# Kernel tuning notes

Hardware: AMD Instinct MI355X
Metric: run time of the kernel (lower is better)

Reference implementation:

```python
import jax, jax.numpy as jnp
import numpy as np

B, S, D, H, FF = 8, 1024, 2048, 16, 8192
Dh = D // H
EPS = 1e-5

def _layernorm(x, g, b):
    m = jnp.mean(x, axis=-1, keepdims=True)
    v = jnp.mean(jnp.square(x - m), axis=-1, keepdims=True)
    return (x - m) / jnp.sqrt(v + EPS) * g + b

def setup_inputs() -> dict:
    key = jax.random.key(0)
    ks = jax.random.split(key, 12)
    sc_d = 1.0 / np.sqrt(D)
    sc_ff = 1.0 / np.sqrt(FF)
    return {
        "x": jax.random.normal(ks[0], (B, S, D), dtype=jnp.float32),
        "mask": jnp.ones((S, S), dtype=jnp.int32),
        "Wq": jax.random.normal(ks[1], (D, D), dtype=jnp.float32) * sc_d,
        "bq": jnp.zeros((D,), dtype=jnp.float32),
        "Wk": jax.random.normal(ks[2], (D, D), dtype=jnp.float32) * sc_d,
        "bk": jnp.zeros((D,), dtype=jnp.float32),
        "Wv": jax.random.normal(ks[3], (D, D), dtype=jnp.float32) * sc_d,
        "bv": jnp.zeros((D,), dtype=jnp.float32),
        "Wo": jax.random.normal(ks[4], (D, D), dtype=jnp.float32) * sc_d,
        "bo": jnp.zeros((D,), dtype=jnp.float32),
        "W1": jax.random.normal(ks[5], (FF, D), dtype=jnp.float32) * sc_d,
        "b1": jnp.zeros((FF,), dtype=jnp.float32),
        "W2": jax.random.normal(ks[6], (D, FF), dtype=jnp.float32) * sc_ff,
        "b2": jnp.zeros((D,), dtype=jnp.float32),
        "g1": jnp.ones((D,), dtype=jnp.float32),
        "be1": jnp.zeros((D,), dtype=jnp.float32),
        "g2": jnp.ones((D,), dtype=jnp.float32),
        "be2": jnp.zeros((D,), dtype=jnp.float32),
    }

def reference(x, mask, Wq, bq, Wk, bk, Wv, bv, Wo, bo, W1, b1, W2, b2, g1, be1, g2, be2):
    # --- multi-head attention (chunk along d_model == reshape to heads) ---
    q = (x @ Wq.T + bq).reshape(B, S, H, Dh)
    k = (x @ Wk.T + bk).reshape(B, S, H, Dh)
    v = (x @ Wv.T + bv).reshape(B, S, H, Dh)
    score = jnp.einsum('bqhd,bkhd->bhqk', q, k) / jnp.sqrt(jnp.float32(Dh))
    score = jnp.where(mask == 0, jnp.float32(-1e9), score)
    attn = jax.nn.softmax(score, axis=-1)
    out = jnp.einsum('bhqk,bkhd->bqhd', attn, v).reshape(B, S, D)
    attn_out = out @ Wo.T + bo
    # --- residual + post-LN ---
    x1 = _layernorm(attn_out + x, g1, be1)
    # --- FFN ---
    h = jax.nn.relu(x1 @ W1.T + b1)
    ffn_out = h @ W2.T + b2
    return _layernorm(ffn_out + x1, g2, be2)
```

## Files before the change

### kernel.cpp

```cpp
#include <hip/hip_runtime.h>
#include <cstdint>
#include <cstddef>


typedef unsigned short u16;
typedef unsigned int   u32;
typedef unsigned long long u64;
typedef __attribute__((ext_vector_type(8))) short short8;
typedef __attribute__((ext_vector_type(4))) float f32x4;

constexpr int Bc  = 8;
constexpr int Sc  = 1024;
constexpr int Dc  = 2048;
constexpr int Hc  = 16;
constexpr int Dhc = 128;
constexpr int FFc = 8192;
constexpr int Mc  = Bc * Sc;

__device__ __forceinline__ u16 f2b(float f) {
  u32 u = __builtin_bit_cast(u32, f);
  u += 0x7fffu + ((u >> 16) & 1u);
  return (u16)(u >> 16);
}
__device__ __forceinline__ u32 pack2(float a, float b) {
  return (u32)f2b(a) | ((u32)f2b(b) << 16);
}
__device__ __forceinline__ void unpack8(uint4 u, float* f) {
  u32 w[4] = {u.x, u.y, u.z, u.w};
#pragma unroll
  for (int i = 0; i < 4; ++i) {
    f[2 * i + 0] = __builtin_bit_cast(float, w[i] << 16);
    f[2 * i + 1] = __builtin_bit_cast(float, w[i] & 0xffff0000u);
  }
}

#define GLOAD_LDS16(gp, lp)                                                    \
  __builtin_amdgcn_global_load_lds(                                            \
      (const __attribute__((address_space(1))) void*)(gp),                     \
      (__attribute__((address_space(3))) void*)(lp), 16, 0, 0)

__global__ __launch_bounds__(256) void cvt_f32_bf16(const float* __restrict__ in,
                                                    u16* __restrict__ out, int n) {
  int i = (blockIdx.x * 256 + threadIdx.x) << 2;
  if (i >= n) return;
  float4 v = *(const float4*)(in + i);
  ushort4 o;
  o.x = f2b(v.x); o.y = f2b(v.y); o.z = f2b(v.z); o.w = f2b(v.w);
  *(ushort4*)(out + i) = o;
}

__global__ __launch_bounds__(256) void mask_bits(const int* __restrict__ mask,
                                                 u64* __restrict__ mb) {
  int t = blockIdx.x * 256 + threadIdx.x;
  int r = t >> 4, wd = t & 15;
  const int* p = mask + (size_t)r * Sc + wd * 64;
  u64 bits = 0;
#pragma unroll 16
  for (int i = 0; i < 64; i += 4) {
    int4 q = *(const int4*)(p + i);
    bits |= (u64)(q.x != 0) << (i + 0);
    bits |= (u64)(q.y != 0) << (i + 1);
    bits |= (u64)(q.z != 0) << (i + 2);
    bits |= (u64)(q.w != 0) << (i + 3);
  }
  mb[t] = bits;
}

template <int MODE>
__global__ __launch_bounds__(512, 2) void gemm256tb(const u16* __restrict__ A,
                                                    const u16* __restrict__ Bt,
                                                    const float* __restrict__ bias,
                                                    u16* __restrict__ C,
                                                    int M, int N, int K) {
  __shared__ u16 Abuf[4][256 * 32];
  __shared__ u16 Bbuf[4][256 * 32];

  const int nbn = N >> 8;
  const int nwg = (M >> 8) * nbn;
  int bid = blockIdx.x;
  int sw = (bid & 7) * (nwg >> 3) + (bid >> 3);
  const int m0 = (sw / nbn) << 8;
  const int n0 = (sw % nbn) << 8;

  const int tid  = threadIdx.x;
  const int lane = tid & 63;
  const int w    = tid >> 6;
  const int wm   = w >> 2;
  const int wn   = w & 3;

  const int rowA = lane & 15;
  const int g4   = lane >> 4;

  const int p16  = lane << 4;
  const int wsw  = p16 ^ (((p16 >> 9) & 1) << 5);
  const int s_rr = wsw >> 6;
  const int s_cc = (wsw & 63) >> 1;

  const int sb = (rowA * 64 + g4 * 16) ^ (((rowA >> 3) & 1) << 5);

  const int NT = K >> 5;

  const u16* Asrc = A  + (size_t)(m0 + w * 32 + s_rr) * K + s_cc;
  const u16* Bsrc = Bt + (size_t)(n0 + w * 32 + s_rr) * K + s_cc;

  auto stage = [&](int tt) {
    int buf = tt & 3;
#pragma unroll
    for (int i = 0; i < 2; ++i)
      GLOAD_LDS16(Asrc + (size_t)i * 16 * K + tt * 32, &Abuf[buf][(2 * w + i) * 512]);
#pragma unroll
    for (int i = 0; i < 2; ++i)
      GLOAD_LDS16(Bsrc + (size_t)i * 16 * K + tt * 32, &Bbuf[buf][(2 * w + i) * 512]);
  };

  auto readF = [&](int tt, short8* aF, short8* bF) {
    int buf = tt & 3;
#pragma unroll
    for (int n = 0; n < 4; ++n)
      bF[n] = *(const short8*)((const char*)&Bbuf[buf][(wn * 4 + n) * 512] + sb);
#pragma unroll
    for (int i = 0; i < 8; ++i)
      aF[i] = *(const short8*)((const char*)&Abuf[buf][(wm * 8 + i) * 512] + sb);
  };

  f32x4 acc[8][4];
#pragma unroll
  for (int m = 0; m < 8; ++m)
#pragma unroll
    for (int n = 0; n < 4; ++n) acc[m][n] = (f32x4){0.f, 0.f, 0.f, 0.f};

  stage(0); stage(1); stage(2);
  asm volatile("s_waitcnt vmcnt(4)" ::: "memory");
  __builtin_amdgcn_s_barrier();

  short8 a0[8], b0[4], a1[8], b1[4];
  readF(0, a0, b0);

  auto body = [&](int t, short8* aC, short8* bC, short8* aN, short8* bN) {
    if (t + 1 < NT) readF(t + 1, aN, bN);
    if (t + 3 < NT) stage(t + 3);
    __builtin_amdgcn_sched_barrier(0);
    __builtin_amdgcn_s_setprio(1);
#pragma unroll
    for (int i = 0; i < 8; ++i)
#pragma unroll
      for (int n = 0; n < 4; ++n)
        acc[i][n] = __builtin_amdgcn_mfma_f32_16x16x32_bf16(aC[i], bC[n], acc[i][n], 0, 0, 0);
    __builtin_amdgcn_s_setprio(0);
    if (t + 3 < NT) { asm volatile("s_waitcnt vmcnt(4)" ::: "memory"); }
    else            { asm volatile("s_waitcnt vmcnt(0)" ::: "memory"); }
    __builtin_amdgcn_s_barrier();
  };

  for (int t = 0; t < NT; t += 2) {
    body(t,     a0, b0, a1, b1);
    body(t + 1, a1, b1, a0, b0);
  }

  const int ci = lane & 15;
  const int ri = g4 << 2;
  float bvv[4];
#pragma unroll
  for (int n = 0; n < 4; ++n) bvv[n] = bias[n0 + wn * 64 + n * 16 + ci];

  if (MODE == 2) {
#pragma unroll
    for (int n = 0; n < 4; ++n) {
      int col = n0 + wn * 64 + n * 16 + ci;
#pragma unroll
      for (int m = 0; m < 8; ++m) {
        int row0 = m0 + wm * 128 + m * 16 + ri;
        ushort4 pk;
        pk.x = f2b(acc[m][n][0] + bvv[n]);
        pk.y = f2b(acc[m][n][1] + bvv[n]);
        pk.z = f2b(acc[m][n][2] + bvv[n]);
        pk.w = f2b(acc[m][n][3] + bvv[n]);
        size_t addr = ((size_t)((row0 >> 10) * Hc + (col >> 7)) * 128 + (col & 127)) * 1024
                      + (row0 & 1023);
        *(ushort4*)(C + addr) = pk;
      }
    }
  } else {
#pragma unroll
    for (int m = 0; m < 8; ++m) {
      int row0 = m0 + wm * 128 + m * 16 + ri;
#pragma unroll
      for (int j = 0; j < 4; ++j) {
        u16* cp = C + (size_t)(row0 + j) * N + n0 + wn * 64 + ci;
#pragma unroll
        for (int n = 0; n < 4; ++n) {
          float v = acc[m][n][j] + bvv[n];
          if (MODE == 1) v = fmaxf(v, 0.f);
          cp[n * 16] = f2b(v);
        }
      }
    }
  }
}

__global__ __launch_bounds__(256, 2) void attn_mfma(
    const u16* __restrict__ qb,
    const u16* __restrict__ kb,
    const u16* __restrict__ vt,
    const u64* __restrict__ mb,
    u16* __restrict__ ob)
{
  __shared__ u16 Ks[64 * 128];
  __shared__ u16 Vts[128 * 64];
  __shared__ u16 Ps[4][32 * 64];

  const int bid = blockIdx.x;
  const int l   = (bid & 7) * 128 + (bid >> 3);
  const int qt  = l & 7;
  const int bh  = l >> 3;
  const int h   = bh & (Hc - 1);
  const int b   = bh >> 4;
  const int q0  = qt * 128;

  const int tid  = threadIdx.x;
  const int lane = tid & 63;
  const int w    = tid >> 6;
  const int rowA = lane & 15;
  const int g4   = lane >> 4;
  const int kq16 = g4 << 3;
  const int ri   = g4 << 2;

  const size_t tokbase = (size_t)b * Sc * Dc + (size_t)h * Dhc;
  const size_t vtbase  = (size_t)bh * 128 * 1024;
  const int qwbase = q0 + w * 32;

  short8 qf[2][4];
#pragma unroll
  for (int m = 0; m < 2; ++m)
#pragma unroll
    for (int kk = 0; kk < 4; ++kk)
      qf[m][kk] = *reinterpret_cast<const short8*>(
          qb + tokbase + (size_t)(qwbase + m * 16 + rowA) * Dc + kk * 32 + kq16);

  f32x4 O[2][8];
#pragma unroll
  for (int m = 0; m < 2; ++m)
#pragma unroll
    for (int n = 0; n < 8; ++n) O[m][n] = (f32x4){0.f, 0.f, 0.f, 0.f};
  float mrow[2][4], lrow[2][4];
#pragma unroll
  for (int m = 0; m < 2; ++m)
#pragma unroll
    for (int j = 0; j < 4; ++j) { mrow[m][j] = -INFINITY; lrow[m][j] = 0.f; }

  const float scale = 0.08838834764831845f;

  for (int kt = 0; kt < Sc / 64; ++kt) {
    const int k0 = kt * 64;
    __syncthreads();
#pragma unroll
    for (int i = 0; i < 4; ++i) {
      int chunk = w * 4 + i;
      int gb = (chunk * 64 + lane) * 16;
      int L  = gb ^ (((gb >> 8) & 7) << 4);
      int row = L >> 8, ce = (L & 255) >> 1;
      GLOAD_LDS16(kb + tokbase + (size_t)(k0 + row) * Dc + ce, &Ks[chunk * 512]);
    }
#pragma unroll
    for (int i = 0; i < 4; ++i) {
      int chunk = w * 4 + i;
      int gb = (chunk * 64 + lane) * 16;
      int L  = gb ^ (((gb >> 7) & 7) << 4);
      int row = L >> 7, ce = (L & 127) >> 1;
      GLOAD_LDS16(vt + vtbase + (size_t)row * 1024 + k0 + ce, &Vts[chunk * 512]);
    }
    __syncthreads();

    f32x4 s[2][4];
#pragma unroll
    for (int m = 0; m < 2; ++m)
#pragma unroll
      for (int n = 0; n < 4; ++n) s[m][n] = (f32x4){0.f, 0.f, 0.f, 0.f};
#pragma unroll
    for (int kk = 0; kk < 4; ++kk) {
      short8 bfk[4];
#pragma unroll
      for (int n = 0; n < 4; ++n) {
        int krow = n * 16 + rowA;
        int by = (krow * 256 + kk * 64 + (g4 << 4)) ^ ((krow & 7) << 4);
        bfk[n] = *reinterpret_cast<const short8*>((const char*)Ks + by);
      }
#pragma unroll
      for (int m = 0; m < 2; ++m)
#pragma unroll
        for (int n = 0; n < 4; ++n)
          s[m][n] = __builtin_amdgcn_mfma_f32_16x16x32_bf16(qf[m][kk], bfk[n], s[m][n], 0, 0, 0);
    }

    float alpha[2][4];
#pragma unroll
    for (int m = 0; m < 2; ++m) {
      u64 wb_[4];
#pragma unroll
      for (int j = 0; j < 4; ++j)
        wb_[j] = mb[(size_t)(qwbase + m * 16 + ri + j) * 16 + kt];
#pragma unroll
      for (int j = 0; j < 4; ++j) {
        float pv[4];
        float mx = -3.0e38f;
#pragma unroll
        for (int n = 0; n < 4; ++n) {
          float x = s[m][n][j] * scale;
          if (!((wb_[j] >> (n * 16 + rowA)) & 1)) x = -1e9f;
          pv[n] = x;
          mx = fmaxf(mx, x);
        }
        mx = fmaxf(mx, __shfl_xor(mx, 1));
        mx = fmaxf(mx, __shfl_xor(mx, 2));
        mx = fmaxf(mx, __shfl_xor(mx, 4));
        mx = fmaxf(mx, __shfl_xor(mx, 8));
        float mnew = fmaxf(mrow[m][j], mx);
        float a = __expf(mrow[m][j] - mnew);
        mrow[m][j] = mnew;
        alpha[m][j] = a;
        float rs = 0.f;
#pragma unroll
        for (int n = 0; n < 4; ++n) {
          float p = __expf(pv[n] - mnew);
          pv[n] = p;
          rs += p;
        }
        rs += __shfl_xor(rs, 1);
        rs += __shfl_xor(rs, 2);
        rs += __shfl_xor(rs, 4);
        rs += __shfl_xor(rs, 8);
        lrow[m][j] = lrow[m][j] * a + rs;
        int prow = m * 16 + ri + j;
#pragma unroll
        for (int n = 0; n < 4; ++n) {
          int by = (prow * 128 + 2 * (n * 16 + rowA)) ^ ((prow & 7) << 4);
          *(u16*)((char*)Ps[w] + by) = f2b(pv[n]);
        }
      }
    }
    asm volatile("s_waitcnt lgkmcnt(0)" ::: "memory");

#pragma unroll
    for (int m = 0; m < 2; ++m)
#pragma unroll
      for (int n = 0; n < 8; ++n)
#pragma unroll
        for (int j = 0; j < 4; ++j) O[m][n][j] *= alpha[m][j];

    short8 pa[2][2];
#pragma unroll
    for (int m = 0; m < 2; ++m)
#pragma unroll
      for (int kk = 0; kk < 2; ++kk) {
        int prow = m * 16 + rowA;
        int by = (prow * 128 + kk * 64 + (g4 << 4)) ^ ((prow & 7) << 4);
        pa[m][kk] = *reinterpret_cast<const short8*>((const char*)Ps[w] + by);
      }
#pragma unroll
    for (int kk = 0; kk < 2; ++kk)
#pragma unroll
      for (int n = 0; n < 8; ++n) {
        int drow = n * 16 + rowA;
        int by = (drow * 128 + kk * 64 + (g4 << 4)) ^ ((drow & 7) << 4);
        short8 bfv = *reinterpret_cast<const short8*>((const char*)Vts + by);
#pragma unroll
        for (int m = 0; m < 2; ++m)
          O[m][n] = __builtin_amdgcn_mfma_f32_16x16x32_bf16(pa[m][kk], bfv, O[m][n], 0, 0, 0);
      }
  }

  float inv[2][4];
#pragma unroll
  for (int m = 0; m < 2; ++m)
#pragma unroll
    for (int j = 0; j < 4; ++j) inv[m][j] = 1.f / lrow[m][j];
#pragma unroll
  for (int m = 0; m < 2; ++m)
#pragma unroll
    for (int n = 0; n < 8; ++n) {
      int dcol = n * 16 + rowA;
#pragma unroll
      for (int j = 0; j < 4; ++j) {
        int qg = qwbase + m * 16 + ri + j;
        ob[tokbase + (size_t)qg * Dc + dcol] = f2b(O[m][n][j] * inv[m][j]);
      }
    }
}

template <int RES_BF16, int OUT_BF16>
__global__ __launch_bounds__(256) void ln_kernel(const u16* __restrict__ a,
                                                 const void* __restrict__ resid,
                                                 const float* __restrict__ g,
                                                 const float* __restrict__ be,
                                                 void* __restrict__ out) {
  int row = blockIdx.x;
  int tid = threadIdx.x;
  int c0  = tid << 3;

  float v[8], vr[8];
  uint4 ua = *(const uint4*)(a + (size_t)row * Dc + c0);
  unpack8(ua, v);
  if (RES_BF16) {
    uint4 ur = *(const uint4*)((const u16*)resid + (size_t)row * Dc + c0);
    unpack8(ur, vr);
  } else {
    const float* rp = (const float*)resid + (size_t)row * Dc + c0;
    float4 f0 = *(const float4*)rp;
    float4 f1 = *(const float4*)(rp + 4);
    vr[0] = f0.x; vr[1] = f0.y; vr[2] = f0.z; vr[3] = f0.w;
    vr[4] = f1.x; vr[5] = f1.y; vr[6] = f1.z; vr[7] = f1.w;
  }

  float s = 0.f, ss = 0.f;
#pragma unroll
  for (int j = 0; j < 8; ++j) {
    v[j] += vr[j];
    s += v[j];
    ss += v[j] * v[j];
  }
#pragma unroll
  for (int off = 32; off; off >>= 1) {
    s  += __shfl_down(s, off);
    ss += __shfl_down(ss, off);
  }
  __shared__ float rs[4], rss[4], stat[2];
  if ((tid & 63) == 0) { rs[tid >> 6] = s; rss[tid >> 6] = ss; }
  __syncthreads();
  if (tid == 0) {
    float t  = rs[0] + rs[1] + rs[2] + rs[3];
    float tt = rss[0] + rss[1] + rss[2] + rss[3];
    float mean = t * (1.f / Dc);
    float var  = tt * (1.f / Dc) - mean * mean;
    stat[0] = mean;
    stat[1] = rsqrtf(var + 1e-5f);
  }
  __syncthreads();
  float mean = stat[0], rstd = stat[1];

  float y[8];
#pragma unroll
  for (int j = 0; j < 8; ++j) y[j] = (v[j] - mean) * rstd * g[c0 + j] + be[c0 + j];

  if (OUT_BF16) {
    uint4 o;
    o.x = pack2(y[0], y[1]); o.y = pack2(y[2], y[3]);
    o.z = pack2(y[4], y[5]); o.w = pack2(y[6], y[7]);
    *(uint4*)((u16*)out + (size_t)row * Dc + c0) = o;
  } else {
    float* op = (float*)out + (size_t)row * Dc + c0;
    *(float4*)op       = (float4){y[0], y[1], y[2], y[3]};
    *(float4*)(op + 4) = (float4){y[4], y[5], y[6], y[7]};
  }
}

extern "C" void kernel_launch(void* const* d_in, const int* in_sizes, int n_in,
                              void* d_out, int out_size, void* d_ws, size_t ws_size,
                              hipStream_t stream) {
  (void)in_sizes; (void)n_in; (void)out_size; (void)ws_size;

  const float* x   = (const float*)d_in[0];
  const int*   mk  = (const int*)d_in[1];
  const float* Wq  = (const float*)d_in[2];
  const float* bq  = (const float*)d_in[3];
  const float* Wk  = (const float*)d_in[4];
  const float* bk  = (const float*)d_in[5];
  const float* Wv  = (const float*)d_in[6];
  const float* bv  = (const float*)d_in[7];
  const float* Wo  = (const float*)d_in[8];
  const float* bo  = (const float*)d_in[9];
  const float* W1  = (const float*)d_in[10];
  const float* b1  = (const float*)d_in[11];
  const float* W2  = (const float*)d_in[12];
  const float* b2  = (const float*)d_in[13];
  const float* g1  = (const float*)d_in[14];
  const float* be1 = (const float*)d_in[15];
  const float* g2  = (const float*)d_in[16];
  const float* be2 = (const float*)d_in[17];
  float* outp = (float*)d_out;

  const size_t R = 16777216;
  u16* xb  = (u16*)d_ws;
  u16* wb  = xb + R;
  u16* qb  = wb + R;
  u16* kb  = qb + R;
  u16* vt  = kb + R;
  u16* ao  = vt + R;
  u64* mbt = (u64*)d_ws;
  u16* ap  = qb;
  u16* x1  = kb;
  u16* hb  = vt;
  u16* ffn = xb;

  auto cvt = [&](const float* src, u16* dst, int n) {
    cvt_f32_bf16<<<dim3((n + 1023) / 1024), dim3(256), 0, stream>>>(src, dst, n);
  };

  cvt(x, xb, Mc * Dc);

  cvt(Wq, wb, Dc * Dc);
  gemm256tb<0><<<dim3(32 * 8), dim3(512), 0, stream>>>(xb, wb, bq, qb, Mc, Dc, Dc);
  cvt(Wk, wb, Dc * Dc);
  gemm256tb<0><<<dim3(32 * 8), dim3(512), 0, stream>>>(xb, wb, bk, kb, Mc, Dc, Dc);
  cvt(Wv, wb, Dc * Dc);
  gemm256tb<2><<<dim3(32 * 8), dim3(512), 0, stream>>>(xb, wb, bv, vt, Mc, Dc, Dc);

  mask_bits<<<dim3(64), dim3(256), 0, stream>>>(mk, mbt);

  attn_mfma<<<dim3(Bc * Hc * (Sc / 128)), dim3(256), 0, stream>>>(qb, kb, vt, mbt, ao);

  cvt(Wo, wb, Dc * Dc);
  gemm256tb<0><<<dim3(32 * 8), dim3(512), 0, stream>>>(ao, wb, bo, ap, Mc, Dc, Dc);
  ln_kernel<0, 1><<<dim3(Mc), dim3(256), 0, stream>>>(ap, x, g1, be1, x1);

  cvt(W1, wb, FFc * Dc);
  gemm256tb<1><<<dim3(32 * 32), dim3(512), 0, stream>>>(x1, wb, b1, hb, Mc, FFc, Dc);
  cvt(W2, wb, Dc * FFc);
  gemm256tb<0><<<dim3(32 * 8), dim3(512), 0, stream>>>(hb, wb, b2, ffn, Mc, Dc, FFc);
  ln_kernel<1, 0><<<dim3(Mc), dim3(256), 0, stream>>>(ffn, x1, g2, be2, outp);
}
```

Measured before the change: 1.046 ms.

## Fuse Q/K/V projections into one GEMM and streamline staging pointers

```diff
diff --git a/kernel.cpp b/kernel.cpp
--- a/kernel.cpp
+++ b/kernel.cpp
@@ -70,6 +70,8 @@
 __global__ __launch_bounds__(512, 2) void gemm256tb(const u16* __restrict__ A,
                                                     const u16* __restrict__ Bt,
                                                     const float* __restrict__ bias,
+                                                    const float* __restrict__ bias2,
+                                                    const float* __restrict__ bias3,
                                                     u16* __restrict__ C,
                                                     int M, int N, int K) {
   __shared__ u16 Abuf[4][256 * 32];
@@ -100,17 +102,16 @@
 
   const int NT = K >> 5;
 
-  const u16* Asrc = A  + (size_t)(m0 + w * 32 + s_rr) * K + s_cc;
-  const u16* Bsrc = Bt + (size_t)(n0 + w * 32 + s_rr) * K + s_cc;
-
-  auto stage = [&](int tt) {
+  const u16* aP = A  + (size_t)(m0 + w * 32 + s_rr) * K + s_cc;
+  const u16* bP = Bt + (size_t)(n0 + w * 32 + s_rr) * K + s_cc;
+  const size_t rstep = (size_t)16 * K;
+
+  auto stage = [&](int tt, const u16* ap, const u16* bp) {
     int buf = tt & 3;
-#pragma unroll
-    for (int i = 0; i < 2; ++i)
-      GLOAD_LDS16(Asrc + (size_t)i * 16 * K + tt * 32, &Abuf[buf][(2 * w + i) * 512]);
-#pragma unroll
-    for (int i = 0; i < 2; ++i)
-      GLOAD_LDS16(Bsrc + (size_t)i * 16 * K + tt * 32, &Bbuf[buf][(2 * w + i) * 512]);
+    GLOAD_LDS16(ap,         &Abuf[buf][(2 * w + 0) * 512]);
+    GLOAD_LDS16(ap + rstep, &Abuf[buf][(2 * w + 1) * 512]);
+    GLOAD_LDS16(bp,         &Bbuf[buf][(2 * w + 0) * 512]);
+    GLOAD_LDS16(bp + rstep, &Bbuf[buf][(2 * w + 1) * 512]);
   };
 
   auto readF = [&](int tt, short8* aF, short8* bF) {
@@ -129,7 +130,10 @@
 #pragma unroll
     for (int n = 0; n < 4; ++n) acc[m][n] = (f32x4){0.f, 0.f, 0.f, 0.f};
 
-  stage(0); stage(1); stage(2);
+  stage(0, aP, bP);
+  stage(1, aP + 32, bP + 32);
+  stage(2, aP + 64, bP + 64);
+  aP += 96; bP += 96;
   asm volatile("s_waitcnt vmcnt(4)" ::: "memory");
   __builtin_amdgcn_s_barrier();
 
@@ -138,8 +142,7 @@
 
   auto body = [&](int t, short8* aC, short8* bC, short8* aN, short8* bN) {
     if (t + 1 < NT) readF(t + 1, aN, bN);
-    if (t + 3 < NT) stage(t + 3);
-    __builtin_amdgcn_sched_barrier(0);
+    if (t + 3 < NT) { stage(t + 3, aP, bP); aP += 32; bP += 32; }
     __builtin_amdgcn_s_setprio(1);
 #pragma unroll
     for (int i = 0; i < 8; ++i)
@@ -159,28 +162,51 @@
 
   const int ci = lane & 15;
   const int ri = g4 << 2;
-  float bvv[4];
-#pragma unroll
-  for (int n = 0; n < 4; ++n) bvv[n] = bias[n0 + wn * 64 + n * 16 + ci];
-
-  if (MODE == 2) {
-#pragma unroll
-    for (int n = 0; n < 4; ++n) {
-      int col = n0 + wn * 64 + n * 16 + ci;
+
+  if (MODE == 3) {
+    const int cb   = n0 + wn * 64;
+    const int seg  = cb >> 11;
+    const int cseg = cb & 2047;
+    const float* bp_ = (seg == 0) ? bias : (seg == 1) ? bias2 : bias3;
+    float bvv[4];
+#pragma unroll
+    for (int n = 0; n < 4; ++n) bvv[n] = bp_[cseg + n * 16 + ci];
+    if (seg < 2) {
+      u16* Cs = C + (size_t)seg * Mc * Dc;
 #pragma unroll
       for (int m = 0; m < 8; ++m) {
         int row0 = m0 + wm * 128 + m * 16 + ri;
-        ushort4 pk;
-        pk.x = f2b(acc[m][n][0] + bvv[n]);
-        pk.y = f2b(acc[m][n][1] + bvv[n]);
-        pk.z = f2b(acc[m][n][2] + bvv[n]);
-        pk.w = f2b(acc[m][n][3] + bvv[n]);
-        size_t addr = ((size_t)((row0 >> 10) * Hc + (col >> 7)) * 128 + (col & 127)) * 1024
-                      + (row0 & 1023);
-        *(ushort4*)(C + addr) = pk;
+#pragma unroll
+        for (int j = 0; j < 4; ++j) {
+          u16* cp = Cs + (size_t)(row0 + j) * Dc + cseg + ci;
+#pragma unroll
+          for (int n = 0; n < 4; ++n)
+            cp[n * 16] = f2b(acc[m][n][j] + bvv[n]);
+        }
+      }
+    } else {
+      u16* Cv = C + (size_t)2 * Mc * Dc;
+#pragma unroll
+      for (int n = 0; n < 4; ++n) {
+        int col = cseg + n * 16 + ci;
+#pragma unroll
+        for (int m = 0; m < 8; ++m) {
+          int row0 = m0 + wm * 128 + m * 16 + ri;
+          ushort4 pk;
+          pk.x = f2b(acc[m][n][0] + bvv[n]);
+          pk.y = f2b(acc[m][n][1] + bvv[n]);
+          pk.z = f2b(acc[m][n][2] + bvv[n]);
+          pk.w = f2b(acc[m][n][3] + bvv[n]);
+          size_t addr = ((size_t)((row0 >> 10) * Hc + (col >> 7)) * 128 + (col & 127)) * 1024
+                        + (row0 & 1023);
+          *(ushort4*)(Cv + addr) = pk;
+        }
       }
     }
   } else {
+    float bvv[4];
+#pragma unroll
+    for (int n = 0; n < 4; ++n) bvv[n] = bias[n0 + wn * 64 + n * 16 + ci];
 #pragma unroll
     for (int m = 0; m < 8; ++m) {
       int row0 = m0 + wm * 128 + m * 16 + ri;
@@ -479,42 +505,48 @@
   float* outp = (float*)d_out;
 
   const size_t R = 16777216;
-  u16* xb  = (u16*)d_ws;
-  u16* wb  = xb + R;
-  u16* qb  = wb + R;
-  u16* kb  = qb + R;
-  u16* vt  = kb + R;
-  u16* ao  = vt + R;
-  u64* mbt = (u64*)d_ws;
-  u16* ap  = qb;
-  u16* x1  = kb;
-  u16* hb  = vt;
-  u16* ffn = xb;
+  u16* xb   = (u16*)d_ws;
+  u16* wqkv = xb + R;
+  u64* mbt  = (u64*)(wqkv + 13 * 1024 * 1024);
+  u16* qb   = xb + 2 * R;
+  u16* ao   = xb + 5 * R;
+  u16* wst6 = xb + 6 * R;
+  u16* x1   = xb + 6 * R;
+  u16* ap   = xb + 7 * R;
+  u16* w1s  = xb;
+  u16* hb   = xb + 2 * R;
+  u16* w2s  = xb + 7 * R;
+  u16* ffn  = wqkv;
+
+  const size_t MD = (size_t)Mc * Dc;
 
   auto cvt = [&](const float* src, u16* dst, int n) {
     cvt_f32_bf16<<<dim3((n + 1023) / 1024), dim3(256), 0, stream>>>(src, dst, n);
   };
 
   cvt(x, xb, Mc * Dc);
-
-  cvt(Wq, wb, Dc * Dc);
-  gemm256tb<0><<<dim3(32 * 8), dim3(512), 0, stream>>>(xb, wb, bq, qb, Mc, Dc, Dc);
-  cvt(Wk, wb, Dc * Dc);
-  gemm256tb<0><<<dim3(32 * 8), dim3(512), 0, stream>>>(xb, wb, bk, kb, Mc, Dc, Dc);
-  cvt(Wv, wb, Dc * Dc);
-  gemm256tb<2><<<dim3(32 * 8), dim3(512), 0, stream>>>(xb, wb, bv, vt, Mc, Dc, Dc);
+  cvt(Wq, wqkv,               Dc * Dc);
+  cvt(Wk, wqkv + Dc * Dc,     Dc * Dc);
+  cvt(Wv, wqkv + 2 * Dc * Dc, Dc * Dc);
+
+  gemm256tb<3><<<dim3(32 * 24), dim3(512), 0, stream>>>(xb, wqkv, bq, bk, bv,
+                                                        qb, Mc, 3 * Dc, Dc);
 
   mask_bits<<<dim3(64), dim3(256), 0, stream>>>(mk, mbt);
 
-  attn_mfma<<<dim3(Bc * Hc * (Sc / 128)), dim3(256), 0, stream>>>(qb, kb, vt, mbt, ao);
-
-  cvt(Wo, wb, Dc * Dc);
-  gemm256tb<0><<<dim3(32 * 8), dim3(512), 0, stream>>>(ao, wb, bo, ap, Mc, Dc, Dc);
+  attn_mfma<<<dim3(Bc * Hc * (Sc / 128)), dim3(256), 0, stream>>>(
+      qb, qb + MD, qb + 2 * MD, mbt, ao);
+
+  cvt(Wo, wst6, Dc * Dc);
+  gemm256tb<0><<<dim3(32 * 8), dim3(512), 0, stream>>>(ao, wst6, bo, bo, bo,
+                                                       ap, Mc, Dc, Dc);
   ln_kernel<0, 1><<<dim3(Mc), dim3(256), 0, stream>>>(ap, x, g1, be1, x1);
 
-  cvt(W1, wb, FFc * Dc);
-  gemm256tb<1><<<dim3(32 * 32), dim3(512), 0, stream>>>(x1, wb, b1, hb, Mc, FFc, Dc);
-  cvt(W2, wb, Dc * FFc);
-  gemm256tb<0><<<dim3(32 * 8), dim3(512), 0, stream>>>(hb, wb, b2, ffn, Mc, Dc, FFc);
+  cvt(W1, w1s, FFc * Dc);
+  gemm256tb<1><<<dim3(32 * 32), dim3(512), 0, stream>>>(x1, w1s, b1, b1, b1,
+                                                        hb, Mc, FFc, Dc);
+  cvt(W2, w2s, Dc * FFc);
+  gemm256tb<0><<<dim3(32 * 8), dim3(512), 0, stream>>>(hb, w2s, b2, b2, b2,
+                                                       ffn, Mc, Dc, FFc);
   ln_kernel<1, 0><<<dim3(Mc), dim3(256), 0, stream>>>(ffn, x1, g2, be2, outp);
 }
```

Result: no change. 1.050 ms (+0.4%).
